# Kernel tuning notes

Hardware: AMD Instinct MI355X
Metric: run time of the kernel (lower is better)

## Reference

```python
import jax, jax.numpy as jnp
import numpy as np

# ---- static configuration (mirrors module init kwargs) ----
RADIUS = 8.0
MAX_NEIGHBORS = 32          # max_num_neighbors_threshold
MAX_REP = (2, 2, 0)         # static: rep = min(ceil(radius*inv_min_dist), threshold) = 2 for a1,a2; pbc[2]=False -> 0
B, N_ATOMS = 32, 128
CELL_EDGE = 4.0


def _unit_cells():
    # torch.cartesian_prod over arange(-rep, rep+1) per dim; pbc z disabled -> single 0
    ax = [np.arange(-r, r + 1, dtype=np.float32) for r in MAX_REP]
    g = np.stack(np.meshgrid(*ax, indexing='ij'), axis=-1).reshape(-1, 3)
    return jnp.asarray(g)  # [C, 3], C = 5*5*1 = 25


def setup_inputs() -> dict:
    key = jax.random.key(0)
    k1, k2 = jax.random.split(key)
    # near-cubic cells ~4A with small perturbation (keeps rep clamped at threshold=2)
    cell = (CELL_EDGE * jnp.eye(3, dtype=jnp.float32)[None] +
            0.05 * jax.random.normal(k2, (B, 3, 3), dtype=jnp.float32))
    # atoms at fractional coords in [0,1): pos = frac @ cell
    frac = jax.random.uniform(k1, (B, N_ATOMS, 3), dtype=jnp.float32)
    pos = jnp.einsum('bnf,bfk->bnk', frac, cell)
    return {'pos': pos, 'cell': cell}


def reference(pos, cell):
    """PBC radius-graph construction (gen_edges_from_batch), padded form.

    Candidate edges live on a fixed grid [B, i, j, c]: i = index1 (center atom),
    j = index2 (neighbor), c = periodic image. Returns:
      edge_dist       [B,N,N,C] f32  distance (0 where edge invalid)
      edge_cell_type  [B,N,N,C] i32  linearized cell-offset id (0 where invalid)
      edge_mask       [B,N,N,C] bool edge survives radius + self + kNN truncation
      num_neighbors_image [B]   i32  per-image edge counts (clamped), as in torch
    """
    u = _unit_cells()                         # [C,3]
    C = u.shape[0]
    # pbc offsets: offset_c = u_c @ cell_b  (matches cell_offsets.bmm(cell))
    off = jnp.einsum('ci,bik->bck', u, cell)  # [B,C,3]

    # distance vectors: pos[index2] - pos[index1] + offset (get_pbc_distances convention)
    dvec = (pos[:, None, :, None, :] - pos[:, :, None, None, :]
            + off[:, None, None, :, :])       # [B,N,N,C,3]
    d2 = jnp.sum(dvec * dvec, axis=-1)        # [B,N,N,C]

    within = (d2 <= RADIUS * RADIUS) & (d2 > 1e-4)

    # --- sort-based neighbor truncation per center atom i (get_max_neighbors_mask) ---
    num_atoms = B * N_ATOMS
    rows = jnp.where(within, d2, jnp.inf).reshape(num_atoms, N_ATOMS * C)
    order = jnp.argsort(rows, axis=1)         # stable: ties keep (j,c) order as torch
    ranks = jnp.argsort(order, axis=1)        # inverse permutation = rank of each cand
    keep = (ranks < MAX_NEIGHBORS).reshape(B, N_ATOMS, N_ATOMS, C) & within

    # per-image clamped neighbor counts (segment_csr of clamped segment_coo)
    num_nb = jnp.sum(within, axis=(2, 3)).astype(jnp.int32)          # [B,N]
    num_neighbors_image = jnp.sum(jnp.minimum(num_nb, MAX_NEIGHBORS), axis=1)

    safe_d2 = jnp.where(keep, d2, 1.0)
    edge_dist = jnp.where(keep, jnp.sqrt(safe_d2), 0.0)

    # linearized cell type: (offsets + max_rep) . [nr1*nr2, nr1, 1] with nr = 2*rep+1
    nr = np.array([2 * r + 1 for r in MAX_REP])
    mults = jnp.asarray([nr[1] * nr[2], nr[1], 1], dtype=jnp.int32)  # matches torch code
    ct = jnp.sum((u.astype(jnp.int32) + jnp.asarray(MAX_REP, jnp.int32)) * mults, axis=-1)  # [C]
    edge_cell_type = jnp.where(keep, ct[None, None, None, :], 0).astype(jnp.int32)

    return edge_dist, edge_cell_type, keep, num_neighbors_image
```

## Files before the change

kernel.cpp:

```cpp
#include <hip/hip_runtime.h>
#include <math.h>
#include <stdint.h>

#define NATOMS   128
#define NCELLS   25
#define NCAND    (NATOMS * NCELLS)
#define MAXNB    32
#define R2       64.0f
#define BLK      256
#define KEYCAP   256

__global__ __launch_bounds__(BLK) void graph_kernel(
    const float* __restrict__ pos, const float* __restrict__ cell,
    float* __restrict__ out_dist, float* __restrict__ out_ctype,
    float* __restrict__ out_mask, float* __restrict__ ws_counts)
{
    __shared__ float s_pos[NATOMS * 3];
    __shared__ float s_ctr[3];
    __shared__ float s_off[NCELLS * 3];
    __shared__ float s_d2[NCAND];
    __shared__ unsigned s_hist[256];
    __shared__ unsigned s_scan[256];
    __shared__ unsigned long long s_keys[KEYCAP];
    __shared__ unsigned s_cnt;
    __shared__ int s_binsel;
    __shared__ int s_need;
    __shared__ unsigned long long s_K;

    const int bi  = blockIdx.x;
    const int b   = bi >> 7;
    const int tid = threadIdx.x;

    for (int t = tid; t < NATOMS * 3; t += BLK)
        s_pos[t] = pos[b * (NATOMS * 3) + t];
    if (tid < 3) s_ctr[tid] = pos[bi * 3 + tid];
    if (tid < NCELLS * 3) {
        int c = tid / 3, k = tid - c * 3;
        float ux = (float)(c / 5 - 2);
        float uy = (float)(c % 5 - 2);
        float c0 = cell[b * 9 + 0 + k];
        float c1 = cell[b * 9 + 3 + k];
        s_off[tid] = __fadd_rn(__fmul_rn(ux, c0), __fmul_rn(uy, c1));
    }
    s_hist[tid] = 0;
    if (tid == 0) { s_cnt = 0; s_binsel = -1; s_need = 0; s_K = ~0ULL; }
    __syncthreads();

    for (int f = tid; f < NCAND; f += BLK) {
        int j = f / NCELLS;
        int c = f - j * NCELLS;
        float dx = __fadd_rn(__fsub_rn(s_pos[j*3+0], s_ctr[0]), s_off[c*3+0]);
        float dy = __fadd_rn(__fsub_rn(s_pos[j*3+1], s_ctr[1]), s_off[c*3+1]);
        float dz = __fadd_rn(__fsub_rn(s_pos[j*3+2], s_ctr[2]), s_off[c*3+2]);
        float d2 = __fadd_rn(__fadd_rn(__fmul_rn(dx,dx), __fmul_rn(dy,dy)),
                             __fmul_rn(dz,dz));
        bool within = (d2 <= R2) && (d2 > 1e-4f);
        s_d2[f] = within ? d2 : __builtin_inff();
        if (within) {
            int bin = (int)(d2 * 4.0f);
            if (bin > 255) bin = 255;
            atomicAdd(&s_hist[bin], 1u);
        }
    }
    __syncthreads();

    const unsigned h = s_hist[tid];
    s_scan[tid] = h;
    __syncthreads();
    #pragma unroll
    for (int off = 1; off < 256; off <<= 1) {
        unsigned v = s_scan[tid];
        unsigned add = (tid >= off) ? s_scan[tid - off] : 0u;
        __syncthreads();
        s_scan[tid] = v + add;
        __syncthreads();
    }
    const unsigned cum_incl = s_scan[tid];
    const unsigned cum_excl = cum_incl - h;
    if (tid == 255) {
        int tot = (int)cum_incl;
        ws_counts[bi] = (float)(tot < MAXNB ? tot : MAXNB);
    }
    if (h > 0 && cum_excl < MAXNB && cum_incl >= MAXNB) {
        s_binsel = tid;
        s_need   = MAXNB - (int)cum_excl;
    }
    __syncthreads();

    const int binsel = s_binsel;
    if (binsel >= 0) {
        for (int f = tid; f < NCAND; f += BLK) {
            float d2 = s_d2[f];
            if (d2 <= R2) {
                int bin = (int)(d2 * 4.0f);
                if (bin > 255) bin = 255;
                if (bin == binsel) {
                    unsigned idx = atomicAdd(&s_cnt, 1u);
                    if (idx < KEYCAP)
                        s_keys[idx] = ((unsigned long long)__float_as_uint(d2) << 32)
                                      | (unsigned)f;
                }
            }
        }
        __syncthreads();
        const int m = (int)s_cnt;
        const int need = s_need;
        if (m <= KEYCAP) {
            for (int p = tid; p < m; p += BLK) {
                unsigned long long kp = s_keys[p];
                int r = 0;
                for (int q = 0; q < m; q++) r += (s_keys[q] < kp);
                if (r == need - 1) s_K = kp;
            }
        } else {
            for (int f = tid; f < NCAND; f += BLK) {
                float d2 = s_d2[f];
                if (d2 <= R2) {
                    int bin = (int)(d2 * 4.0f);
                    if (bin > 255) bin = 255;
                    if (bin == binsel) {
                        unsigned long long kf =
                            ((unsigned long long)__float_as_uint(d2) << 32) | (unsigned)f;
                        int r = 0;
                        for (int q = 0; q < NCAND; q++) {
                            float dq = s_d2[q];
                            if (dq <= R2) {
                                int bq = (int)(dq * 4.0f);
                                if (bq > 255) bq = 255;
                                if (bq == binsel) {
                                    unsigned long long kq =
                                        ((unsigned long long)__float_as_uint(dq) << 32)
                                        | (unsigned)q;
                                    r += (kq < kf);
                                }
                            }
                        }
                        if (r == need - 1) s_K = kf;
                    }
                }
            }
        }
        __syncthreads();
    }
    const unsigned long long K = s_K;

    const long long base = (long long)bi * NCAND;
    float4* o0 = (float4*)(out_dist  + base);
    float4* o1 = (float4*)(out_ctype + base);
    float4* o2 = (float4*)(out_mask  + base);
    for (int v = tid; v < NCAND / 4; v += BLK) {
        float4 dq = ((const float4*)s_d2)[v];
        float d[4] = {dq.x, dq.y, dq.z, dq.w};
        float4 r0, r1, r2;
        float* p0 = &r0.x; float* p1 = &r1.x; float* p2 = &r2.x;
        #pragma unroll
        for (int e = 0; e < 4; e++) {
            int f = v * 4 + e;
            float d2 = d[e];
            bool within = (d2 <= R2);
            unsigned long long key =
                ((unsigned long long)__float_as_uint(d2) << 32) | (unsigned)f;
            bool keep = within && (key <= K);
            int c = f % NCELLS;
            p0[e] = keep ? sqrtf(d2) : 0.0f;
            p1[e] = keep ? (float)(5 * (c / 5) + 5 * (c % 5)) : 0.0f;
            p2[e] = keep ? 1.0f : 0.0f;
        }
        o0[v] = r0; o1[v] = r1; o2[v] = r2;
    }
}

__global__ __launch_bounds__(64) void reduce_counts(
    const float* __restrict__ ws_counts, float* __restrict__ out_nb)
{
    int b = blockIdx.x;
    int t = threadIdx.x;
    float v = ws_counts[b * NATOMS + t] + ws_counts[b * NATOMS + 64 + t];
    for (int o = 32; o; o >>= 1) v += __shfl_down(v, o);
    if (t == 0) out_nb[b] = v;
}

extern "C" void kernel_launch(void* const* d_in, const int* in_sizes, int n_in,
                              void* d_out, int out_size, void* d_ws, size_t ws_size,
                              hipStream_t stream) {
    const float* pos  = (const float*)d_in[0];
    const float* cell = (const float*)d_in[1];
    float* out = (float*)d_out;
    const long long E = 32LL * NATOMS * NATOMS * NCELLS;
    float* out_dist  = out;
    float* out_ct    = out + E;
    float* out_mask  = out + 2 * E;
    float* out_nb    = out + 3 * E;
    float* ws = (float*)d_ws;

    hipLaunchKernelGGL(graph_kernel, dim3(32 * NATOMS), dim3(BLK), 0, stream,
                       pos, cell, out_dist, out_ct, out_mask, ws);
    hipLaunchKernelGGL(reduce_counts, dim3(32), dim3(64), 0, stream,
                       ws, out_nb);
}
```

Baseline: 170.2 us.

## Use finer histogram over near range, wave-shuffle scan, and skip selection when few neighbors

Replaces the 256-entry shared-memory Hillis-Steele scan with a wave-level shuffle scan. The first pass builds a finer histogram (16 bins per unit d2) covering only d2 < 16, with a fallback rebuild over the full range. Counts are reduced with shuffles, and threshold selection is skipped entirely when an atom has at most 32 neighbors. Positions and offsets are stored as float4, candidates are iterated cell-major for conflict-free reads, and cell types come from a table. This adds complexity and a possible second histogram pass, and the smaller key capacity raises the chance of hitting the slow fallback.

```diff
diff --git a/kernel.cpp b/kernel.cpp
--- a/kernel.cpp
+++ b/kernel.cpp
@@ -8,103 +8,147 @@
 #define MAXNB    32
 #define R2       64.0f
 #define BLK      256
-#define KEYCAP   256
+#define KEYCAP   128
 
 __global__ __launch_bounds__(BLK) void graph_kernel(
     const float* __restrict__ pos, const float* __restrict__ cell,
     float* __restrict__ out_dist, float* __restrict__ out_ctype,
     float* __restrict__ out_mask, float* __restrict__ ws_counts)
 {
-    __shared__ float s_pos[NATOMS * 3];
-    __shared__ float s_ctr[3];
-    __shared__ float s_off[NCELLS * 3];
-    __shared__ float s_d2[NCAND];
+    __shared__ float4 s_pos4[NATOMS];
+    __shared__ float4 s_off4[NCELLS];
+    __shared__ float  s_ct[NCELLS];
+    __shared__ float  s_ctr[3];
+    __shared__ float  s_d2[NCAND];
     __shared__ unsigned s_hist[256];
-    __shared__ unsigned s_scan[256];
+    __shared__ unsigned s_wtot[4];
+    __shared__ int s_wred[4];
     __shared__ unsigned long long s_keys[KEYCAP];
     __shared__ unsigned s_cnt;
-    __shared__ int s_binsel;
-    __shared__ int s_need;
+    __shared__ int s_binsel, s_need, s_tot, s_att;
     __shared__ unsigned long long s_K;
 
-    const int bi  = blockIdx.x;
-    const int b   = bi >> 7;
-    const int tid = threadIdx.x;
-
-    for (int t = tid; t < NATOMS * 3; t += BLK)
-        s_pos[t] = pos[b * (NATOMS * 3) + t];
-    if (tid < 3) s_ctr[tid] = pos[bi * 3 + tid];
-    if (tid < NCELLS * 3) {
-        int c = tid / 3, k = tid - c * 3;
+    const int bi   = blockIdx.x;
+    const int b    = bi >> 7;
+    const int tid  = threadIdx.x;
+    const int lane = tid & 63;
+    const int w    = tid >> 6;
+
+    if (tid < NATOMS) {
+        const float* p = pos + (b * NATOMS + tid) * 3;
+        s_pos4[tid] = make_float4(p[0], p[1], p[2], 0.0f);
+    }
+    if (tid >= NATOMS && tid < NATOMS + 3)
+        s_ctr[tid - NATOMS] = pos[bi * 3 + (tid - NATOMS)];
+    if (tid >= 160 && tid < 160 + NCELLS) {
+        int c = tid - 160;
         float ux = (float)(c / 5 - 2);
         float uy = (float)(c % 5 - 2);
-        float c0 = cell[b * 9 + 0 + k];
-        float c1 = cell[b * 9 + 3 + k];
-        s_off[tid] = __fadd_rn(__fmul_rn(ux, c0), __fmul_rn(uy, c1));
-    }
-    s_hist[tid] = 0;
-    if (tid == 0) { s_cnt = 0; s_binsel = -1; s_need = 0; s_K = ~0ULL; }
+        float ox = __fadd_rn(__fmul_rn(ux, cell[b*9+0]), __fmul_rn(uy, cell[b*9+3]));
+        float oy = __fadd_rn(__fmul_rn(ux, cell[b*9+1]), __fmul_rn(uy, cell[b*9+4]));
+        float oz = __fadd_rn(__fmul_rn(ux, cell[b*9+2]), __fmul_rn(uy, cell[b*9+5]));
+        s_off4[c] = make_float4(ox, oy, oz, 0.0f);
+        s_ct[c] = (float)(5 * (c / 5) + 5 * (c % 5));
+    }
+    s_hist[tid] = 0u;
+    if (tid == 0) { s_cnt = 0; s_binsel = -1; s_need = 0; s_att = 0; s_K = ~0ULL; }
     __syncthreads();
 
-    for (int f = tid; f < NCAND; f += BLK) {
-        int j = f / NCELLS;
-        int c = f - j * NCELLS;
-        float dx = __fadd_rn(__fsub_rn(s_pos[j*3+0], s_ctr[0]), s_off[c*3+0]);
-        float dy = __fadd_rn(__fsub_rn(s_pos[j*3+1], s_ctr[1]), s_off[c*3+1]);
-        float dz = __fadd_rn(__fsub_rn(s_pos[j*3+2], s_ctr[2]), s_off[c*3+2]);
+    const float cx = s_ctr[0], cy = s_ctr[1], cz = s_ctr[2];
+
+    int local = 0;
+    for (int g = tid; g < NCAND; g += BLK) {
+        int c = g >> 7;
+        int j = g & 127;
+        float4 p = s_pos4[j];
+        float4 o = s_off4[c];
+        float dx = __fadd_rn(__fsub_rn(p.x, cx), o.x);
+        float dy = __fadd_rn(__fsub_rn(p.y, cy), o.y);
+        float dz = __fadd_rn(__fsub_rn(p.z, cz), o.z);
         float d2 = __fadd_rn(__fadd_rn(__fmul_rn(dx,dx), __fmul_rn(dy,dy)),
                              __fmul_rn(dz,dz));
         bool within = (d2 <= R2) && (d2 > 1e-4f);
+        int f = j * NCELLS + c;
         s_d2[f] = within ? d2 : __builtin_inff();
         if (within) {
-            int bin = (int)(d2 * 4.0f);
-            if (bin > 255) bin = 255;
-            atomicAdd(&s_hist[bin], 1u);
-        }
-    }
+            local++;
+            if (d2 < 16.0f)
+                atomicAdd(&s_hist[(int)(d2 * 16.0f)], 1u);
+        }
+    }
+    for (int o = 32; o; o >>= 1) local += __shfl_down(local, o);
+    if (lane == 0) s_wred[w] = local;
     __syncthreads();
-
-    const unsigned h = s_hist[tid];
-    s_scan[tid] = h;
+    if (tid == 0) {
+        int tot = s_wred[0] + s_wred[1] + s_wred[2] + s_wred[3];
+        s_tot = tot;
+        ws_counts[bi] = (float)(tot < MAXNB ? tot : MAXNB);
+    }
     __syncthreads();
-    #pragma unroll
-    for (int off = 1; off < 256; off <<= 1) {
-        unsigned v = s_scan[tid];
-        unsigned add = (tid >= off) ? s_scan[tid - off] : 0u;
+
+    if (s_tot > MAXNB) {
+        for (int att = 0; att < 2 && s_binsel < 0; att++) {
+            if (att == 1) {
+                s_hist[tid] = 0u;
+                __syncthreads();
+                for (int v = tid; v < NCAND / 4; v += BLK) {
+                    float4 dq = ((const float4*)s_d2)[v];
+                    #pragma unroll
+                    for (int e = 0; e < 4; e++) {
+                        float d2 = (&dq.x)[e];
+                        if (d2 < 64.5f) {
+                            int bin = (int)(d2 * 4.0f);
+                            if (bin > 255) bin = 255;
+                            atomicAdd(&s_hist[bin], 1u);
+                        }
+                    }
+                }
+                __syncthreads();
+            }
+            unsigned h = s_hist[tid];
+            int v = (int)h;
+            #pragma unroll
+            for (int off = 1; off < 64; off <<= 1) {
+                int u = __shfl_up(v, off, 64);
+                if (lane >= off) v += u;
+            }
+            if (lane == 63) s_wtot[w] = (unsigned)v;
+            __syncthreads();
+            unsigned pre = 0;
+            for (int ww = 0; ww < w; ww++) pre += s_wtot[ww];
+            unsigned htot = s_wtot[0] + s_wtot[1] + s_wtot[2] + s_wtot[3];
+            unsigned ci = (unsigned)v + pre, ce = ci - h;
+            if (htot >= MAXNB && h > 0 && ce < MAXNB && ci >= MAXNB) {
+                s_binsel = tid;
+                s_need   = MAXNB - (int)ce;
+                s_att    = att;
+            }
+            __syncthreads();
+        }
+
+        const int   binsel = s_binsel;
+        const float sc  = s_att ? 4.0f  : 16.0f;
+        const float lim = s_att ? 64.5f : 16.0f;
+        for (int v = tid; v < NCAND / 4; v += BLK) {
+            float4 dq = ((const float4*)s_d2)[v];
+            #pragma unroll
+            for (int e = 0; e < 4; e++) {
+                float d2 = (&dq.x)[e];
+                if (d2 < lim) {
+                    int bin = (int)(d2 * sc);
+                    if (bin > 255) bin = 255;
+                    if (bin == binsel) {
+                        unsigned idx = atomicAdd(&s_cnt, 1u);
+                        if (idx < KEYCAP)
+                            s_keys[idx] =
+                                ((unsigned long long)__float_as_uint(d2) << 32)
+                                | (unsigned)(v * 4 + e);
+                    }
+                }
+            }
+        }
         __syncthreads();
-        s_scan[tid] = v + add;
-        __syncthreads();
-    }
-    const unsigned cum_incl = s_scan[tid];
-    const unsigned cum_excl = cum_incl - h;
-    if (tid == 255) {
-        int tot = (int)cum_incl;
-        ws_counts[bi] = (float)(tot < MAXNB ? tot : MAXNB);
-    }
-    if (h > 0 && cum_excl < MAXNB && cum_incl >= MAXNB) {
-        s_binsel = tid;
-        s_need   = MAXNB - (int)cum_excl;
-    }
-    __syncthreads();
-
-    const int binsel = s_binsel;
-    if (binsel >= 0) {
-        for (int f = tid; f < NCAND; f += BLK) {
-            float d2 = s_d2[f];
-            if (d2 <= R2) {
-                int bin = (int)(d2 * 4.0f);
-                if (bin > 255) bin = 255;
-                if (bin == binsel) {
-                    unsigned idx = atomicAdd(&s_cnt, 1u);
-                    if (idx < KEYCAP)
-                        s_keys[idx] = ((unsigned long long)__float_as_uint(d2) << 32)
-                                      | (unsigned)f;
-                }
-            }
-        }
-        __syncthreads();
-        const int m = (int)s_cnt;
-        const int need = s_need;
+        const int m = (int)s_cnt, need = s_need;
         if (m <= KEYCAP) {
             for (int p = tid; p < m; p += BLK) {
                 unsigned long long kp = s_keys[p];
@@ -115,8 +159,8 @@
         } else {
             for (int f = tid; f < NCAND; f += BLK) {
                 float d2 = s_d2[f];
-                if (d2 <= R2) {
-                    int bin = (int)(d2 * 4.0f);
+                if (d2 < lim) {
+                    int bin = (int)(d2 * sc);
                     if (bin > 255) bin = 255;
                     if (bin == binsel) {
                         unsigned long long kf =
@@ -124,8 +168,8 @@
                         int r = 0;
                         for (int q = 0; q < NCAND; q++) {
                             float dq = s_d2[q];
-                            if (dq <= R2) {
-                                int bq = (int)(dq * 4.0f);
+                            if (dq < lim) {
+                                int bq = (int)(dq * sc);
                                 if (bq > 255) bq = 255;
                                 if (bq == binsel) {
                                     unsigned long long kq =
@@ -150,21 +194,20 @@
     float4* o2 = (float4*)(out_mask  + base);
     for (int v = tid; v < NCAND / 4; v += BLK) {
         float4 dq = ((const float4*)s_d2)[v];
-        float d[4] = {dq.x, dq.y, dq.z, dq.w};
+        int f0 = v * 4;
+        int c0 = f0 % NCELLS;
         float4 r0, r1, r2;
-        float* p0 = &r0.x; float* p1 = &r1.x; float* p2 = &r2.x;
         #pragma unroll
         for (int e = 0; e < 4; e++) {
-            int f = v * 4 + e;
-            float d2 = d[e];
+            float d2 = (&dq.x)[e];
+            int ce = c0 + e; if (ce >= NCELLS) ce -= NCELLS;
             bool within = (d2 <= R2);
             unsigned long long key =
-                ((unsigned long long)__float_as_uint(d2) << 32) | (unsigned)f;
+                ((unsigned long long)__float_as_uint(d2) << 32) | (unsigned)(f0 + e);
             bool keep = within && (key <= K);
-            int c = f % NCELLS;
-            p0[e] = keep ? sqrtf(d2) : 0.0f;
-            p1[e] = keep ? (float)(5 * (c / 5) + 5 * (c % 5)) : 0.0f;
-            p2[e] = keep ? 1.0f : 0.0f;
+            (&r0.x)[e] = keep ? sqrtf(d2) : 0.0f;
+            (&r1.x)[e] = keep ? s_ct[ce] : 0.0f;
+            (&r2.x)[e] = keep ? 1.0f : 0.0f;
         }
         o0[v] = r0; o1[v] = r1; o2[v] = r2;
     }
```

Result: no change. 167.9 us (-1.4%).
